# Kernel tuning notes

Measured on AMD Instinct MI355X. Metric: run time of the kernel, lower is better.

## Reference

```python
import jax, jax.numpy as jnp
import numpy as np
import math

B, S, D, H, FF, L = 8, 1024, 1024, 8, 4096, 2
DK = D // H
NEG = -1e32
EPS = 1e-5


def _cosine_pe(seq_len, d_model):
    pos = jnp.arange(seq_len, dtype=jnp.float32)[:, None]
    div = jnp.exp(jnp.arange(0, d_model, 2, dtype=jnp.float32) * (-(math.log(10000.0) / d_model)))
    pe = jnp.zeros((seq_len, d_model), dtype=jnp.float32)
    pe = pe.at[:, 0::2].set(jnp.sin(pos * div))
    pe = pe.at[:, 1::2].set(jnp.cos(pos * div))
    return pe


def setup_inputs() -> dict:
    key = jax.random.key(0)
    ks = jax.random.split(key, 12)
    sc = 0.02
    g = lambda k, shape: (jax.random.normal(k, shape, jnp.float32) * sc)
    return {
        "q_embed": jax.random.normal(ks[0], (B, S, D), jnp.float32),
        "qa_embed": jax.random.normal(ks[1], (B, S, D), jnp.float32),
        "pos_emb": _cosine_pe(S, D),
        "Wk": g(ks[2], (L, D, D)), "bk": jnp.zeros((L, D), jnp.float32),
        "Wv": g(ks[3], (L, D, D)), "bv": jnp.zeros((L, D), jnp.float32),
        "Wo": g(ks[4], (L, D, D)), "bo": jnp.zeros((L, D), jnp.float32),
        "ln1_g": jnp.ones((L, D), jnp.float32), "ln1_b": jnp.zeros((L, D), jnp.float32),
        "W1": g(ks[5], (L, FF, D)), "b1": jnp.zeros((L, FF), jnp.float32),
        "W2": g(ks[6], (L, D, FF)), "b2": jnp.zeros((L, D), jnp.float32),
        "ln2_g": jnp.ones((L, D), jnp.float32), "ln2_b": jnp.zeros((L, D), jnp.float32),
    }


def _layernorm(x, g, b):
    m = jnp.mean(x, axis=-1, keepdims=True)
    v = jnp.mean(jnp.square(x - m), axis=-1, keepdims=True)
    return (x - m) * jax.lax.rsqrt(v + EPS) * g + b


def _mha(x, y, Wk, bk, Wv, bv, Wo, bo, allow):
    # kq_same=1: q and k both come from k_linear applied to x (query==key input)
    k = (jnp.einsum('bsd,od->bso', x, Wk) + bk).reshape(B, S, H, DK).transpose(0, 2, 1, 3)
    q = k  # identical projection and identical input
    v = (jnp.einsum('bsd,od->bso', y, Wv) + bv).reshape(B, S, H, DK).transpose(0, 2, 1, 3)
    scores = jnp.einsum('bhqd,bhkd->bhqk', q, k) / math.sqrt(DK)
    scores = jnp.where(allow, scores, NEG)  # masked_fill(mask==0, -1e32)
    attn = jax.nn.softmax(scores, axis=-1)
    attn = attn.at[:, :, 0, :].set(0.0)  # zero_pad: first query row zeroed
    out = jnp.einsum('bhqk,bhkd->bhqd', attn, v)
    out = out.transpose(0, 2, 1, 3).reshape(B, S, D)
    return jnp.einsum('bsd,od->bso', out, Wo) + bo


def reference(q_embed, qa_embed, pos_emb, Wk, bk, Wv, bv, Wo, bo,
              ln1_g, ln1_b, W1, b1, W2, b2, ln2_g, ln2_b):
    x = q_embed + pos_emb[None]
    y = qa_embed + pos_emb[None]
    # strictly-lower-triangular allowed positions (triu(k=0)==0)
    allow = jnp.tril(jnp.ones((S, S), dtype=bool), -1)[None, None]
    for l in range(L):
        q2 = _mha(x, x, y, Wk[l], bk[l], Wv[l], bv[l], Wo[l], bo[l], allow) if False else _mha(x, y, Wk[l], bk[l], Wv[l], bv[l], Wo[l], bo[l], allow)
        x = _layernorm(x + q2, ln1_g[l], ln1_b[l])
        ff = jnp.einsum('bsf,df->bsd', jax.nn.relu(jnp.einsum('bsd,fd->bsf', x, W1[l]) + b1[l]), W2[l]) + b2[l]
        x = _layernorm(x + ff, ln2_g[l], ln2_b[l])
    return x
```

## Files before the change

### kernel.cpp

```cpp
#include <hip/hip_runtime.h>
#include <hip/hip_bf16.h>
#include <cstdint>
#include <cstddef>

#define B_  8
#define S_  1024
#define D_  1024
#define H_  8
#define FF_ 4096
#define L_  2
#define DK_ 128

typedef __bf16 bf16x8 __attribute__((ext_vector_type(8)));
typedef float  f32x4  __attribute__((ext_vector_type(4)));

__device__ __forceinline__ unsigned short f2bf(float f) {
    union { float f; uint32_t u; } v; v.f = f;
    uint32_t r = v.u + 0x7fffu + ((v.u >> 16) & 1u);
    return (unsigned short)(r >> 16);
}
__device__ __forceinline__ float bf2f(unsigned short u) {
    union { uint32_t u; float f; } v; v.u = ((uint32_t)u) << 16; return v.f;
}

__global__ __launch_bounds__(256) void init_xy(
    const float* __restrict__ qe, const float* __restrict__ qa,
    const float* __restrict__ pe,
    unsigned short* __restrict__ xb, unsigned short* __restrict__ yb)
{
    int i = (blockIdx.x * 256 + threadIdx.x) * 4;
    int pi = i & (S_ * D_ - 1);
    float4 q = *(const float4*)(qe + i);
    float4 a = *(const float4*)(qa + i);
    float4 p = *(const float4*)(pe + pi);
    ushort4 xo; xo.x = f2bf(q.x + p.x); xo.y = f2bf(q.y + p.y);
    xo.z = f2bf(q.z + p.z); xo.w = f2bf(q.w + p.w);
    ushort4 yo; yo.x = f2bf(a.x + p.x); yo.y = f2bf(a.y + p.y);
    yo.z = f2bf(a.z + p.z); yo.w = f2bf(a.w + p.w);
    *(ushort4*)(xb + i) = xo;
    *(ushort4*)(yb + i) = yo;
}

__global__ __launch_bounds__(256) void cvt_bf16(
    const float* __restrict__ in, unsigned short* __restrict__ out)
{
    int i = (blockIdx.x * 256 + threadIdx.x) * 4;
    float4 f = *(const float4*)(in + i);
    ushort4 o; o.x = f2bf(f.x); o.y = f2bf(f.y); o.z = f2bf(f.z); o.w = f2bf(f.w);
    *(ushort4*)(out + i) = o;
}

template<bool RELU, int OMODE>
__global__ __launch_bounds__(256) void gemm_bt(
    const unsigned short* __restrict__ A, const unsigned short* __restrict__ W,
    const float* __restrict__ bias, void* __restrict__ Cout,
    int M, int N, int K)
{
    __shared__ unsigned short sA[2][128][64];
    __shared__ unsigned short sW[2][128][64];

    const int tid  = threadIdx.x;
    const int lane = tid & 63;
    const int w    = tid >> 6;
    const int l16  = lane & 15;
    const int quad = lane >> 4;
    const int m0 = blockIdx.y * 128;
    const int n0 = blockIdx.x * 128;
    const int rw = (w >> 1) * 64;
    const int cw = (w & 1) * 64;

    const int srow   = lane >> 3;
    const int schunk = lane & 7;

    auto stage = [&](int k0, int buf) {
        #pragma unroll
        for (int i = 0; i < 4; ++i) {
            int r0  = w * 32 + i * 8;
            int row = r0 + srow;
            int gc  = schunk ^ (row & 7);
            const unsigned short* ga = A + (size_t)(m0 + row) * K + k0 + gc * 8;
            const unsigned short* gw = W + (size_t)(n0 + row) * K + k0 + gc * 8;
            __builtin_amdgcn_global_load_lds(
                (const __attribute__((address_space(1))) unsigned int*)ga,
                (__attribute__((address_space(3))) unsigned int*)&sA[buf][r0][0], 16, 0, 0);
            __builtin_amdgcn_global_load_lds(
                (const __attribute__((address_space(1))) unsigned int*)gw,
                (__attribute__((address_space(3))) unsigned int*)&sW[buf][r0][0], 16, 0, 0);
        }
    };

    f32x4 acc[4][4] = {};
    const int NK = K >> 6;
    int cur = 0;
    stage(0, 0);

    for (int kt = 0; kt < NK; ++kt) {
        __syncthreads();
        if (kt + 1 < NK) stage((kt + 1) << 6, cur ^ 1);

        #pragma unroll
        for (int ks = 0; ks < 2; ++ks) {
            bf16x8 af[4], wf[4];
            #pragma unroll
            for (int t = 0; t < 4; ++t) {
                int arow = rw + t * 16 + l16;
                int achk = (ks * 4 + quad) ^ (arow & 7);
                af[t] = *(const bf16x8*)&sA[cur][arow][achk * 8];
                int wrow = cw + t * 16 + l16;
                int wchk = (ks * 4 + quad) ^ (wrow & 7);
                wf[t] = *(const bf16x8*)&sW[cur][wrow][wchk * 8];
            }
            #pragma unroll
            for (int it = 0; it < 4; ++it)
                #pragma unroll
                for (int jt = 0; jt < 4; ++jt)
                    acc[it][jt] = __builtin_amdgcn_mfma_f32_16x16x32_bf16(
                        af[it], wf[jt], acc[it][jt], 0, 0, 0);
        }
        cur ^= 1;
    }

    #pragma unroll
    for (int it = 0; it < 4; ++it)
        #pragma unroll
        for (int jt = 0; jt < 4; ++jt) {
            int row = m0 + rw + it * 16 + quad * 4;
            int col = n0 + cw + jt * 16 + l16;
            float bcol = bias[col];
            float v[4];
            #pragma unroll
            for (int r = 0; r < 4; ++r) {
                v[r] = acc[it][jt][r] + bcol;
                if (RELU) v[r] = fmaxf(v[r], 0.0f);
            }
            if (OMODE == 1) {
                #pragma unroll
                for (int r = 0; r < 4; ++r)
                    ((unsigned short*)Cout)[(size_t)(row + r) * N + col] = f2bf(v[r]);
            } else {
                int key = row & (S_ - 1);
                int bb  = row >> 10;
                int hh  = col >> 7, dim = col & (DK_ - 1);
                unsigned short* dst = (unsigned short*)Cout
                    + ((size_t)(bb * H_ + hh) * DK_ + dim) * S_ + key;
                ushort4 o4; o4.x = f2bf(v[0]); o4.y = f2bf(v[1]);
                o4.z = f2bf(v[2]); o4.w = f2bf(v[3]);
                *(ushort4*)dst = o4;
            }
        }
}

template<bool RELU>
__global__ __launch_bounds__(512, 2) void gemm_bt8(
    const unsigned short* __restrict__ A, const unsigned short* __restrict__ W,
    const float* __restrict__ bias, unsigned short* __restrict__ Cout,
    int M, int N, int K)
{
    __shared__ unsigned short sA[2][256][64];
    __shared__ unsigned short sB[2][256][64];

    const int tid  = threadIdx.x;
    const int lane = tid & 63;
    const int w    = tid >> 6;
    const int l16  = lane & 15;
    const int quad = lane >> 4;
    const int wr   = w >> 2;
    const int wc   = w & 3;

    const int nwg = gridDim.x * gridDim.y;
    const int bid = blockIdx.y * gridDim.x + blockIdx.x;
    const int sb  = (bid & 7) * (nwg >> 3) + (bid >> 3);
    const int m0  = (sb / gridDim.x) * 256;
    const int n0  = (sb % gridDim.x) * 256;

    const int srow8 = lane >> 3;
    const int schk  = (lane & 7) ^ srow8;

    auto stA = [&](int i, int buf, int k0) {
        int r0 = i * 64 + w * 8;
        const unsigned short* g = A + (size_t)(m0 + r0 + srow8) * K + k0 + schk * 8;
        __builtin_amdgcn_global_load_lds(
            (const __attribute__((address_space(1))) unsigned int*)g,
            (__attribute__((address_space(3))) unsigned int*)&sA[buf][r0][0], 16, 0, 0);
    };
    auto stB = [&](int i, int buf, int k0) {
        int r0 = i * 64 + w * 8;
        const unsigned short* g = W + (size_t)(n0 + r0 + srow8) * K + k0 + schk * 8;
        __builtin_amdgcn_global_load_lds(
            (const __attribute__((address_space(1))) unsigned int*)g,
            (__attribute__((address_space(3))) unsigned int*)&sB[buf][r0][0], 16, 0, 0);
    };
    auto rdA = [&](int buf, int t, int ks) {
        int row = wr * 128 + t * 16 + l16;
        int chk = (ks * 4 + quad) ^ (row & 7);
        return *(const bf16x8*)&sA[buf][row][chk * 8];
    };
    auto rdB = [&](int buf, int j, int ks) {
        int row = wc * 64 + j * 16 + l16;
        int chk = (ks * 4 + quad) ^ (row & 7);
        return *(const bf16x8*)&sB[buf][row][chk * 8];
    };

    f32x4 acc[8][4] = {};
    const int NK = K >> 6;
    int cur = 0;

    stB(0, 0, 0); stB(1, 0, 0); stB(2, 0, 0); stB(3, 0, 0);
    stA(0, 0, 0); stA(2, 0, 0); stA(1, 0, 0); stA(3, 0, 0);
    asm volatile("s_waitcnt vmcnt(2)\n\ts_barrier" ::: "memory");

    for (int kt = 0; kt < NK; ++kt) {
        const bool pref = (kt + 1 < NK);
        const int  k1   = (kt + 1) << 6;
        const int  nb   = cur ^ 1;
        bf16x8 bfr[2][4];
        bf16x8 a0, a1, a2, a3;

        #pragma unroll
        for (int ks = 0; ks < 2; ++ks)
            #pragma unroll
            for (int j = 0; j < 4; ++j) bfr[ks][j] = rdB(cur, j, ks);
        a0 = rdA(cur, 0, 0); a1 = rdA(cur, 0, 1);
        a2 = rdA(cur, 1, 0); a3 = rdA(cur, 1, 1);
        if (pref) { stB(0, nb, k1); stB(1, nb, k1); }
        __builtin_amdgcn_s_setprio(1);
        #pragma unroll
        for (int j = 0; j < 4; ++j) {
            acc[0][j] = __builtin_amdgcn_mfma_f32_16x16x32_bf16(a0, bfr[0][j], acc[0][j], 0, 0, 0);
            acc[1][j] = __builtin_amdgcn_mfma_f32_16x16x32_bf16(a2, bfr[0][j], acc[1][j], 0, 0, 0);
        }
        #pragma unroll
        for (int j = 0; j < 4; ++j) {
            acc[0][j] = __builtin_amdgcn_mfma_f32_16x16x32_bf16(a1, bfr[1][j], acc[0][j], 0, 0, 0);
            acc[1][j] = __builtin_amdgcn_mfma_f32_16x16x32_bf16(a3, bfr[1][j], acc[1][j], 0, 0, 0);
        }
        __builtin_amdgcn_s_setprio(0);
        asm volatile("s_barrier" ::: "memory");

        a0 = rdA(cur, 2, 0); a1 = rdA(cur, 2, 1);
        a2 = rdA(cur, 3, 0); a3 = rdA(cur, 3, 1);
        if (pref) { stB(2, nb, k1); stB(3, nb, k1); }
        __builtin_amdgcn_s_setprio(1);
        #pragma unroll
        for (int j = 0; j < 4; ++j) {
            acc[2][j] = __builtin_amdgcn_mfma_f32_16x16x32_bf16(a0, bfr[0][j], acc[2][j], 0, 0, 0);
            acc[3][j] = __builtin_amdgcn_mfma_f32_16x16x32_bf16(a2, bfr[0][j], acc[3][j], 0, 0, 0);
        }
        #pragma unroll
        for (int j = 0; j < 4; ++j) {
            acc[2][j] = __builtin_amdgcn_mfma_f32_16x16x32_bf16(a1, bfr[1][j], acc[2][j], 0, 0, 0);
            acc[3][j] = __builtin_amdgcn_mfma_f32_16x16x32_bf16(a3, bfr[1][j], acc[3][j], 0, 0, 0);
        }
        __builtin_amdgcn_s_setprio(0);
        if (pref) asm volatile("s_waitcnt vmcnt(4)\n\ts_barrier" ::: "memory");
        else      asm volatile("s_waitcnt vmcnt(0)\n\ts_barrier" ::: "memory");

        a0 = rdA(cur, 4, 0); a1 = rdA(cur, 4, 1);
        a2 = rdA(cur, 5, 0); a3 = rdA(cur, 5, 1);
        if (pref) { stA(0, nb, k1); stA(2, nb, k1); }
        __builtin_amdgcn_s_setprio(1);
        #pragma unroll
        for (int j = 0; j < 4; ++j) {
            acc[4][j] = __builtin_amdgcn_mfma_f32_16x16x32_bf16(a0, bfr[0][j], acc[4][j], 0, 0, 0);
            acc[5][j] = __builtin_amdgcn_mfma_f32_16x16x32_bf16(a2, bfr[0][j], acc[5][j], 0, 0, 0);
        }
        #pragma unroll
        for (int j = 0; j < 4; ++j) {
            acc[4][j] = __builtin_amdgcn_mfma_f32_16x16x32_bf16(a1, bfr[1][j], acc[4][j], 0, 0, 0);
            acc[5][j] = __builtin_amdgcn_mfma_f32_16x16x32_bf16(a3, bfr[1][j], acc[5][j], 0, 0, 0);
        }
        __builtin_amdgcn_s_setprio(0);
        asm volatile("s_barrier" ::: "memory");

        a0 = rdA(cur, 6, 0); a1 = rdA(cur, 6, 1);
        a2 = rdA(cur, 7, 0); a3 = rdA(cur, 7, 1);
        if (pref) { stA(1, nb, k1); stA(3, nb, k1); }
        __builtin_amdgcn_s_setprio(1);
        #pragma unroll
        for (int j = 0; j < 4; ++j) {
            acc[6][j] = __builtin_amdgcn_mfma_f32_16x16x32_bf16(a0, bfr[0][j], acc[6][j], 0, 0, 0);
            acc[7][j] = __builtin_amdgcn_mfma_f32_16x16x32_bf16(a2, bfr[0][j], acc[7][j], 0, 0, 0);
        }
        #pragma unroll
        for (int j = 0; j < 4; ++j) {
            acc[6][j] = __builtin_amdgcn_mfma_f32_16x16x32_bf16(a1, bfr[1][j], acc[6][j], 0, 0, 0);
            acc[7][j] = __builtin_amdgcn_mfma_f32_16x16x32_bf16(a3, bfr[1][j], acc[7][j], 0, 0, 0);
        }
        __builtin_amdgcn_s_setprio(0);
        asm volatile("s_waitcnt vmcnt(2)\n\ts_barrier" ::: "memory");
        cur = nb;
    }

    #pragma unroll
    for (int t = 0; t < 8; ++t)
        #pragma unroll
        for (int j = 0; j < 4; ++j) {
            int row = m0 + wr * 128 + t * 16 + quad * 4;
            int col = n0 + wc * 64 + j * 16 + l16;
            float bcol = bias[col];
            #pragma unroll
            for (int r = 0; r < 4; ++r) {
                float v = acc[t][j][r] + bcol;
                if (RELU) v = fmaxf(v, 0.0f);
                Cout[(size_t)(row + r) * N + col] = f2bf(v);
            }
        }
}

__global__ __launch_bounds__(256) void attn_mfma(
    const unsigned short* __restrict__ Kbuf, const unsigned short* __restrict__ Vtbuf,
    unsigned short* __restrict__ Obuf)
{
    __shared__ unsigned short sK[2][64][128];
    __shared__ unsigned short sVt[2][128][64];
    __shared__ unsigned short sP[4][16][72];

    const int tid  = threadIdx.x;
    const int lane = tid & 63;
    const int w    = tid >> 6;
    const int l16  = lane & 15;
    const int quad = lane >> 4;
    const int pa   = blockIdx.x;
    const int bh   = blockIdx.y;
    const int b    = bh >> 3, h = bh & 7;
    const unsigned short* KB  = Kbuf  + ((size_t)b * S_) * D_ + h * DK_;
    const unsigned short* VTB = Vtbuf + (size_t)bh * DK_ * S_;

    const float scale = 0.08838834764831845f;

    auto stage = [&](int kt, int buf) {
        #pragma unroll
        for (int i = 0; i < 4; ++i) {
            int r0  = w * 16 + i * 4;
            int row = r0 + (lane >> 4);
            int c   = (lane & 15) ^ (row & 15);
            const unsigned short* g = KB + (size_t)(kt * 64 + row) * D_ + c * 8;
            __builtin_amdgcn_global_load_lds(
                (const __attribute__((address_space(1))) unsigned int*)g,
                (__attribute__((address_space(3))) unsigned int*)&sK[buf][r0][0], 16, 0, 0);
        }
        #pragma unroll
        for (int i = 0; i < 4; ++i) {
            int r0  = w * 32 + i * 8;
            int row = r0 + (lane >> 3);
            int c   = (lane & 7) ^ (row & 7);
            const unsigned short* g = VTB + (size_t)row * S_ + kt * 64 + c * 8;
            __builtin_amdgcn_global_load_lds(
                (const __attribute__((address_space(1))) unsigned int*)g,
                (__attribute__((address_space(3))) unsigned int*)&sVt[buf][r0][0], 16, 0, 0);
        }
    };

    #pragma unroll
    for (int half = 0; half < 2; ++half) {
        const int qt = half == 0 ? (15 - pa) : pa;
        const int q0 = qt * 64;

        bf16x8 qf[4];
        {
            const unsigned short* qrow = KB + (size_t)(q0 + w * 16 + l16) * D_ + quad * 8;
            #pragma unroll
            for (int ks = 0; ks < 4; ++ks)
                qf[ks] = *(const bf16x8*)(qrow + ks * 32);
        }

        f32x4 Oacc[8] = {};
        float m_run[4] = {-1e30f, -1e30f, -1e30f, -1e30f};
        float l_run[4] = {};

        int cur = 0;
        stage(0, cur);

        for (int kt = 0; kt <= qt; ++kt) {
            __syncthreads();
            if (kt < qt) stage(kt + 1, cur ^ 1);

            f32x4 sacc[4];
            #pragma unroll
            for (int nt = 0; nt < 4; ++nt) {
                f32x4 a = {};
                #pragma unroll
                for (int ks = 0; ks < 4; ++ks) {
                    int kr = nt * 16 + l16;
                    int p  = (ks * 4 + quad) ^ (kr & 15);
                    bf16x8 kf = *(const bf16x8*)&sK[cur][kr][p * 8];
                    a = __builtin_amdgcn_mfma_f32_16x16x32_bf16(qf[ks], kf, a, 0, 0, 0);
                }
                sacc[nt] = a;
            }

            const bool diag = (kt == qt);
            #pragma unroll
            for (int nt = 0; nt < 4; ++nt)
                #pragma unroll
                for (int r = 0; r < 4; ++r) {
                    float v = sacc[nt][r] * scale;
                    if (diag) {
                        int nidx = nt * 16 + l16;
                        int midx = w * 16 + quad * 4 + r;
                        if (nidx >= midx) v = -1e30f;
                    }
                    sacc[nt][r] = v;
                }

            float alpha[4];
            #pragma unroll
            for (int r = 0; r < 4; ++r) {
                float mx = fmaxf(fmaxf(sacc[0][r], sacc[1][r]), fmaxf(sacc[2][r], sacc[3][r]));
                mx = fmaxf(mx, __shfl_xor(mx, 1));
                mx = fmaxf(mx, __shfl_xor(mx, 2));
                mx = fmaxf(mx, __shfl_xor(mx, 4));
                mx = fmaxf(mx, __shfl_xor(mx, 8));
                float mn = fmaxf(m_run[r], mx);
                alpha[r] = __expf(m_run[r] - mn);
                m_run[r] = mn;
            }
            #pragma unroll
            for (int r = 0; r < 4; ++r) {
                float rs = 0.0f;
                #pragma unroll
                for (int nt = 0; nt < 4; ++nt) {
                    float e = __expf(sacc[nt][r] - m_run[r]);
                    sacc[nt][r] = e;
                    rs += e;
                }
                rs += __shfl_xor(rs, 1);
                rs += __shfl_xor(rs, 2);
                rs += __shfl_xor(rs, 4);
                rs += __shfl_xor(rs, 8);
                l_run[r] = l_run[r] * alpha[r] + rs;
            }
            #pragma unroll
            for (int o = 0; o < 8; ++o)
                #pragma unroll
                for (int r = 0; r < 4; ++r)
                    Oacc[o][r] *= alpha[r];

            #pragma unroll
            for (int nt = 0; nt < 4; ++nt)
                #pragma unroll
                for (int r = 0; r < 4; ++r)
                    sP[w][quad * 4 + r][nt * 16 + l16] = f2bf(sacc[nt][r]);

            bf16x8 pf[2];
            #pragma unroll
            for (int ks = 0; ks < 2; ++ks)
                pf[ks] = *(const bf16x8*)&sP[w][l16][ks * 32 + quad * 8];
            #pragma unroll
            for (int nt = 0; nt < 8; ++nt) {
                #pragma unroll
                for (int ks = 0; ks < 2; ++ks) {
                    int vr = nt * 16 + l16;
                    int p  = (ks * 4 + quad) ^ (vr & 7);
                    bf16x8 vf = *(const bf16x8*)&sVt[cur][vr][p * 8];
                    Oacc[nt] = __builtin_amdgcn_mfma_f32_16x16x32_bf16(pf[ks], vf, Oacc[nt], 0, 0, 0);
                }
            }
            cur ^= 1;
        }

        float inv[4];
        #pragma unroll
        for (int r = 0; r < 4; ++r) {
            int m = q0 + w * 16 + quad * 4 + r;
            inv[r] = (l_run[r] > 0.0f && m != 0) ? 1.0f / l_run[r] : 0.0f;
        }
        #pragma unroll
        for (int nt = 0; nt < 8; ++nt)
            #pragma unroll
            for (int r = 0; r < 4; ++r) {
                int m = q0 + w * 16 + quad * 4 + r;
                Obuf[((size_t)b * S_ + m) * D_ + h * DK_ + nt * 16 + l16] =
                    f2bf(Oacc[nt][r] * inv[r]);
            }
    }
}

template<bool FINAL>
__global__ __launch_bounds__(256) void ln_res(
    const unsigned short* __restrict__ xin, const unsigned short* __restrict__ delta,
    const float* __restrict__ g, const float* __restrict__ bta,
    unsigned short* __restrict__ xbout, float* __restrict__ fout)
{
    __shared__ float red1[4], red2[4];
    const int row = blockIdx.x;
    const int tid = threadIdx.x;
    const int c = tid * 4;
    ushort4 xu = *(const ushort4*)(xin + (size_t)row * D_ + c);
    ushort4 du = *(const ushort4*)(delta + (size_t)row * D_ + c);
    float t0 = bf2f(xu.x) + bf2f(du.x), t1 = bf2f(xu.y) + bf2f(du.y);
    float t2 = bf2f(xu.z) + bf2f(du.z), t3 = bf2f(xu.w) + bf2f(du.w);

    float s = t0 + t1 + t2 + t3;
    #pragma unroll
    for (int off = 32; off > 0; off >>= 1) s += __shfl_down(s, off);
    if ((tid & 63) == 0) red1[tid >> 6] = s;
    __syncthreads();
    float mean = (red1[0] + red1[1] + red1[2] + red1[3]) * (1.0f / 1024.0f);

    float e0 = t0 - mean, e1 = t1 - mean, e2 = t2 - mean, e3 = t3 - mean;
    float ss = e0 * e0 + e1 * e1 + e2 * e2 + e3 * e3;
    #pragma unroll
    for (int off = 32; off > 0; off >>= 1) ss += __shfl_down(ss, off);
    if ((tid & 63) == 0) red2[tid >> 6] = ss;
    __syncthreads();
    float var = (red2[0] + red2[1] + red2[2] + red2[3]) * (1.0f / 1024.0f);
    float rstd = rsqrtf(var + 1e-5f);

    float4 gv = *(const float4*)(g + c);
    float4 bv = *(const float4*)(bta + c);
    float o0 = e0 * rstd * gv.x + bv.x;
    float o1 = e1 * rstd * gv.y + bv.y;
    float o2 = e2 * rstd * gv.z + bv.z;
    float o3 = e3 * rstd * gv.w + bv.w;
    if (FINAL) {
        *(float4*)(fout + (size_t)row * D_ + c) = make_float4(o0, o1, o2, o3);
    } else {
        ushort4 ob; ob.x = f2bf(o0); ob.y = f2bf(o1); ob.z = f2bf(o2); ob.w = f2bf(o3);
        *(ushort4*)(xbout + (size_t)row * D_ + c) = ob;
    }
}

extern "C" void kernel_launch(void* const* d_in, const int* in_sizes, int n_in,
                              void* d_out, int out_size, void* d_ws, size_t ws_size,
                              hipStream_t stream)
{
    const float* qe   = (const float*)d_in[0];
    const float* qa   = (const float*)d_in[1];
    const float* pe   = (const float*)d_in[2];
    const float* Wk   = (const float*)d_in[3];
    const float* bk   = (const float*)d_in[4];
    const float* Wv   = (const float*)d_in[5];
    const float* bv   = (const float*)d_in[6];
    const float* Wo   = (const float*)d_in[7];
    const float* bo   = (const float*)d_in[8];
    const float* ln1g = (const float*)d_in[9];
    const float* ln1b = (const float*)d_in[10];
    const float* W1   = (const float*)d_in[11];
    const float* b1   = (const float*)d_in[12];
    const float* W2   = (const float*)d_in[13];
    const float* b2   = (const float*)d_in[14];
    const float* ln2g = (const float*)d_in[15];
    const float* ln2b = (const float*)d_in[16];

    const size_t BSD = (size_t)B_ * S_ * D_;
    const size_t BSF = (size_t)B_ * S_ * FF_;
    const size_t WDD = (size_t)D_ * D_;
    const size_t WFD = (size_t)FF_ * D_;

    char* p = (char*)d_ws;
    auto take = [&](size_t bytes) { char* r = p; p += (bytes + 255) & ~255ULL; return r; };
    unsigned short* xb    = (unsigned short*)take(BSD * 2);
    unsigned short* yb    = (unsigned short*)take(BSD * 2);
    unsigned short* delta = (unsigned short*)take(BSD * 2);
    char*           uni   = take(BSF * 2);
    unsigned short* Kb    = (unsigned short*)uni;
    unsigned short* Vt    = Kb + BSD;
    unsigned short* attnb = Vt + BSD;
    unsigned short* hb    = (unsigned short*)uni;
    unsigned short* wslot = (unsigned short*)take(WFD * 2);

    init_xy<<<(int)(BSD / 4 / 256), 256, 0, stream>>>(qe, qa, pe, xb, yb);

    const int M = B_ * S_;
    for (int l = 0; l < L_; ++l) {
        cvt_bf16<<<(int)(WDD / 1024), 256, 0, stream>>>(Wk + l * WDD, wslot);
        gemm_bt<false, 1><<<dim3(D_ / 128, M / 128), 256, 0, stream>>>(
            xb, wslot, bk + l * D_, Kb, M, D_, D_);
        cvt_bf16<<<(int)(WDD / 1024), 256, 0, stream>>>(Wv + l * WDD, wslot);
        gemm_bt<false, 2><<<dim3(D_ / 128, M / 128), 256, 0, stream>>>(
            yb, wslot, bv + l * D_, Vt, M, D_, D_);
        attn_mfma<<<dim3(8, B_ * H_), 256, 0, stream>>>(Kb, Vt, attnb);
        cvt_bf16<<<(int)(WDD / 1024), 256, 0, stream>>>(Wo + l * WDD, wslot);
        gemm_bt<false, 1><<<dim3(D_ / 128, M / 128), 256, 0, stream>>>(
            attnb, wslot, bo + l * D_, delta, M, D_, D_);
        ln_res<false><<<M, 256, 0, stream>>>(xb, delta, ln1g + l * D_, ln1b + l * D_, xb, nullptr);
        cvt_bf16<<<(int)(WFD / 1024), 256, 0, stream>>>(W1 + l * WFD, wslot);
        gemm_bt8<true><<<dim3(FF_ / 256, M / 256), 512, 0, stream>>>(
            xb, wslot, b1 + l * FF_, hb, M, FF_, D_);
        cvt_bf16<<<(int)(WFD / 1024), 256, 0, stream>>>(W2 + l * WFD, wslot);
        gemm_bt<false, 1><<<dim3(D_ / 128, M / 128), 256, 0, stream>>>(
            hb, wslot, b2 + l * D_, delta, M, D_, FF_);
        if (l == L_ - 1)
            ln_res<true><<<M, 256, 0, stream>>>(xb, delta, ln2g + l * D_, ln2b + l * D_,
                                               nullptr, (float*)d_out);
        else
            ln_res<false><<<M, 256, 0, stream>>>(xb, delta, ln2g + l * D_, ln2b + l * D_,
                                                xb, nullptr);
    }
}
```

Measured before the change: 830.1 us.

## Replace 128x128 GEMM with 256x128 pipelined 8-wave kernel for N=1024 projections

Adds a gemm_btn kernel that uses a 256x128 tile with 8 waves, split-phase prefetch via global_load_lds, s_setprio around the MFMA bursts, and XCD-aware block swizzling. It replaces the older 128x128 4-wave gemm_bt for the K, V, O and W2 projections, keeping the transposed V output mode. The aim is more reuse per LDS load and better overlap of loads with MFMA on the N=1024 GEMMs. The cost is that the grid shrinks to 256 blocks, which may underfill the CUs.

Result: slower. 872.5 us (+5.1%).

```diff
diff --git a/kernel.cpp b/kernel.cpp
--- a/kernel.cpp
+++ b/kernel.cpp
@@ -50,89 +50,314 @@
     *(ushort4*)(out + i) = o;
 }
 
-template<bool RELU, int OMODE>
-__global__ __launch_bounds__(256) void gemm_bt(
+template<bool RELU>
+__global__ __launch_bounds__(512, 2) void gemm_bt8(
     const unsigned short* __restrict__ A, const unsigned short* __restrict__ W,
-    const float* __restrict__ bias, void* __restrict__ Cout,
+    const float* __restrict__ bias, unsigned short* __restrict__ Cout,
     int M, int N, int K)
 {
-    __shared__ unsigned short sA[2][128][64];
-    __shared__ unsigned short sW[2][128][64];
+    __shared__ unsigned short sA[2][256][64];
+    __shared__ unsigned short sB[2][256][64];
 
     const int tid  = threadIdx.x;
     const int lane = tid & 63;
     const int w    = tid >> 6;
     const int l16  = lane & 15;
     const int quad = lane >> 4;
-    const int m0 = blockIdx.y * 128;
-    const int n0 = blockIdx.x * 128;
-    const int rw = (w >> 1) * 64;
-    const int cw = (w & 1) * 64;
-
-    const int srow   = lane >> 3;
-    const int schunk = lane & 7;
-
-    auto stage = [&](int k0, int buf) {
-        #pragma unroll
-        for (int i = 0; i < 4; ++i) {
-            int r0  = w * 32 + i * 8;
-            int row = r0 + srow;
-            int gc  = schunk ^ (row & 7);
-            const unsigned short* ga = A + (size_t)(m0 + row) * K + k0 + gc * 8;
-            const unsigned short* gw = W + (size_t)(n0 + row) * K + k0 + gc * 8;
-            __builtin_amdgcn_global_load_lds(
-                (const __attribute__((address_space(1))) unsigned int*)ga,
-                (__attribute__((address_space(3))) unsigned int*)&sA[buf][r0][0], 16, 0, 0);
-            __builtin_amdgcn_global_load_lds(
-                (const __attribute__((address_space(1))) unsigned int*)gw,
-                (__attribute__((address_space(3))) unsigned int*)&sW[buf][r0][0], 16, 0, 0);
-        }
-    };
-
-    f32x4 acc[4][4] = {};
+    const int wr   = w >> 2;
+    const int wc   = w & 3;
+
+    const int nwg = gridDim.x * gridDim.y;
+    const int bid = blockIdx.y * gridDim.x + blockIdx.x;
+    const int sb  = (bid & 7) * (nwg >> 3) + (bid >> 3);
+    const int m0  = (sb / gridDim.x) * 256;
+    const int n0  = (sb % gridDim.x) * 256;
+
+    const int srow8 = lane >> 3;
+    const int schk  = (lane & 7) ^ srow8;
+
+    auto stA = [&](int i, int buf, int k0) {
+        int r0 = i * 64 + w * 8;
+        const unsigned short* g = A + (size_t)(m0 + r0 + srow8) * K + k0 + schk * 8;
+        __builtin_amdgcn_global_load_lds(
+            (const __attribute__((address_space(1))) unsigned int*)g,
+            (__attribute__((address_space(3))) unsigned int*)&sA[buf][r0][0], 16, 0, 0);
+    };
+    auto stB = [&](int i, int buf, int k0) {
+        int r0 = i * 64 + w * 8;
+        const unsigned short* g = W + (size_t)(n0 + r0 + srow8) * K + k0 + schk * 8;
+        __builtin_amdgcn_global_load_lds(
+            (const __attribute__((address_space(1))) unsigned int*)g,
+            (__attribute__((address_space(3))) unsigned int*)&sB[buf][r0][0], 16, 0, 0);
+    };
+    auto rdA = [&](int buf, int t, int ks) {
+        int row = wr * 128 + t * 16 + l16;
+        int chk = (ks * 4 + quad) ^ (row & 7);
+        return *(const bf16x8*)&sA[buf][row][chk * 8];
+    };
+    auto rdB = [&](int buf, int j, int ks) {
+        int row = wc * 64 + j * 16 + l16;
+        int chk = (ks * 4 + quad) ^ (row & 7);
+        return *(const bf16x8*)&sB[buf][row][chk * 8];
+    };
+
+    f32x4 acc[8][4] = {};
     const int NK = K >> 6;
     int cur = 0;
-    stage(0, 0);
+
+    stB(0, 0, 0); stB(1, 0, 0); stB(2, 0, 0); stB(3, 0, 0);
+    stA(0, 0, 0); stA(2, 0, 0); stA(1, 0, 0); stA(3, 0, 0);
+    asm volatile("s_waitcnt vmcnt(2)\n\ts_barrier" ::: "memory");
 
     for (int kt = 0; kt < NK; ++kt) {
-        __syncthreads();
-        if (kt + 1 < NK) stage((kt + 1) << 6, cur ^ 1);
-
-        #pragma unroll
-        for (int ks = 0; ks < 2; ++ks) {
-            bf16x8 af[4], wf[4];
-            #pragma unroll
-            for (int t = 0; t < 4; ++t) {
-                int arow = rw + t * 16 + l16;
-                int achk = (ks * 4 + quad) ^ (arow & 7);
-                af[t] = *(const bf16x8*)&sA[cur][arow][achk * 8];
-                int wrow = cw + t * 16 + l16;
-                int wchk = (ks * 4 + quad) ^ (wrow & 7);
-                wf[t] = *(const bf16x8*)&sW[cur][wrow][wchk * 8];
+        const bool pref = (kt + 1 < NK);
+        const int  k1   = (kt + 1) << 6;
+        const int  nb   = cur ^ 1;
+        bf16x8 bfr[2][4];
+        bf16x8 a0, a1, a2, a3;
+
+        #pragma unroll
+        for (int ks = 0; ks < 2; ++ks)
+            #pragma unroll
+            for (int j = 0; j < 4; ++j) bfr[ks][j] = rdB(cur, j, ks);
+        a0 = rdA(cur, 0, 0); a1 = rdA(cur, 0, 1);
+        a2 = rdA(cur, 1, 0); a3 = rdA(cur, 1, 1);
+        if (pref) { stB(0, nb, k1); stB(1, nb, k1); }
+        __builtin_amdgcn_s_setprio(1);
+        #pragma unroll
+        for (int j = 0; j < 4; ++j) {
+            acc[0][j] = __builtin_amdgcn_mfma_f32_16x16x32_bf16(a0, bfr[0][j], acc[0][j], 0, 0, 0);
+            acc[1][j] = __builtin_amdgcn_mfma_f32_16x16x32_bf16(a2, bfr[0][j], acc[1][j], 0, 0, 0);
+        }
+        #pragma unroll
+        for (int j = 0; j < 4; ++j) {
+            acc[0][j] = __builtin_amdgcn_mfma_f32_16x16x32_bf16(a1, bfr[1][j], acc[0][j], 0, 0, 0);
+            acc[1][j] = __builtin_amdgcn_mfma_f32_16x16x32_bf16(a3, bfr[1][j], acc[1][j], 0, 0, 0);
+        }
+        __builtin_amdgcn_s_setprio(0);
+        asm volatile("s_barrier" ::: "memory");
+
+        a0 = rdA(cur, 2, 0); a1 = rdA(cur, 2, 1);
+        a2 = rdA(cur, 3, 0); a3 = rdA(cur, 3, 1);
+        if (pref) { stB(2, nb, k1); stB(3, nb, k1); }
+        __builtin_amdgcn_s_setprio(1);
+        #pragma unroll
+        for (int j = 0; j < 4; ++j) {
+            acc[2][j] = __builtin_amdgcn_mfma_f32_16x16x32_bf16(a0, bfr[0][j], acc[2][j], 0, 0, 0);
+            acc[3][j] = __builtin_amdgcn_mfma_f32_16x16x32_bf16(a2, bfr[0][j], acc[3][j], 0, 0, 0);
+        }
+        #pragma unroll
+        for (int j = 0; j < 4; ++j) {
+            acc[2][j] = __builtin_amdgcn_mfma_f32_16x16x32_bf16(a1, bfr[1][j], acc[2][j], 0, 0, 0);
+            acc[3][j] = __builtin_amdgcn_mfma_f32_16x16x32_bf16(a3, bfr[1][j], acc[3][j], 0, 0, 0);
+        }
+        __builtin_amdgcn_s_setprio(0);
+        if (pref) asm volatile("s_waitcnt vmcnt(4)\n\ts_barrier" ::: "memory");
+        else      asm volatile("s_waitcnt vmcnt(0)\n\ts_barrier" ::: "memory");
+
+        a0 = rdA(cur, 4, 0); a1 = rdA(cur, 4, 1);
+        a2 = rdA(cur, 5, 0); a3 = rdA(cur, 5, 1);
+        if (pref) { stA(0, nb, k1); stA(2, nb, k1); }
+        __builtin_amdgcn_s_setprio(1);
+        #pragma unroll
+        for (int j = 0; j < 4; ++j) {
+            acc[4][j] = __builtin_amdgcn_mfma_f32_16x16x32_bf16(a0, bfr[0][j], acc[4][j], 0, 0, 0);
+            acc[5][j] = __builtin_amdgcn_mfma_f32_16x16x32_bf16(a2, bfr[0][j], acc[5][j], 0, 0, 0);
+        }
+        #pragma unroll
+        for (int j = 0; j < 4; ++j) {
+            acc[4][j] = __builtin_amdgcn_mfma_f32_16x16x32_bf16(a1, bfr[1][j], acc[4][j], 0, 0, 0);
+            acc[5][j] = __builtin_amdgcn_mfma_f32_16x16x32_bf16(a3, bfr[1][j], acc[5][j], 0, 0, 0);
+        }
+        __builtin_amdgcn_s_setprio(0);
+        asm volatile("s_barrier" ::: "memory");
+
+        a0 = rdA(cur, 6, 0); a1 = rdA(cur, 6, 1);
+        a2 = rdA(cur, 7, 0); a3 = rdA(cur, 7, 1);
+        if (pref) { stA(1, nb, k1); stA(3, nb, k1); }
+        __builtin_amdgcn_s_setprio(1);
+        #pragma unroll
+        for (int j = 0; j < 4; ++j) {
+            acc[6][j] = __builtin_amdgcn_mfma_f32_16x16x32_bf16(a0, bfr[0][j], acc[6][j], 0, 0, 0);
+            acc[7][j] = __builtin_amdgcn_mfma_f32_16x16x32_bf16(a2, bfr[0][j], acc[7][j], 0, 0, 0);
+        }
+        #pragma unroll
+        for (int j = 0; j < 4; ++j) {
+            acc[6][j] = __builtin_amdgcn_mfma_f32_16x16x32_bf16(a1, bfr[1][j], acc[6][j], 0, 0, 0);
+            acc[7][j] = __builtin_amdgcn_mfma_f32_16x16x32_bf16(a3, bfr[1][j], acc[7][j], 0, 0, 0);
+        }
+        __builtin_amdgcn_s_setprio(0);
+        asm volatile("s_waitcnt vmcnt(2)\n\ts_barrier" ::: "memory");
+        cur = nb;
+    }
+
+    #pragma unroll
+    for (int t = 0; t < 8; ++t)
+        #pragma unroll
+        for (int j = 0; j < 4; ++j) {
+            int row = m0 + wr * 128 + t * 16 + quad * 4;
+            int col = n0 + wc * 64 + j * 16 + l16;
+            float bcol = bias[col];
+            #pragma unroll
+            for (int r = 0; r < 4; ++r) {
+                float v = acc[t][j][r] + bcol;
+                if (RELU) v = fmaxf(v, 0.0f);
+                Cout[(size_t)(row + r) * N + col] = f2bf(v);
             }
-            #pragma unroll
-            for (int it = 0; it < 4; ++it)
-                #pragma unroll
-                for (int jt = 0; jt < 4; ++jt)
-                    acc[it][jt] = __builtin_amdgcn_mfma_f32_16x16x32_bf16(
-                        af[it], wf[jt], acc[it][jt], 0, 0, 0);
-        }
-        cur ^= 1;
+        }
+}
+
+template<int OMODE>
+__global__ __launch_bounds__(512, 2) void gemm_btn(
+    const unsigned short* __restrict__ A, const unsigned short* __restrict__ W,
+    const float* __restrict__ bias, void* __restrict__ Cout,
+    int M, int N, int K)
+{
+    __shared__ unsigned short sA[2][256][64];
+    __shared__ unsigned short sB[2][128][64];
+
+    const int tid  = threadIdx.x;
+    const int lane = tid & 63;
+    const int w    = tid >> 6;
+    const int l16  = lane & 15;
+    const int quad = lane >> 4;
+    const int wr   = w >> 2;
+    const int wc   = w & 3;
+
+    const int nwg = gridDim.x * gridDim.y;
+    const int bid = blockIdx.y * gridDim.x + blockIdx.x;
+    const int sb  = (bid & 7) * (nwg >> 3) + (bid >> 3);
+    const int m0  = (sb / gridDim.x) * 256;
+    const int n0  = (sb % gridDim.x) * 128;
+
+    const int srow8 = lane >> 3;
+    const int schk  = (lane & 7) ^ srow8;
+
+    auto stA = [&](int i, int buf, int k0) {
+        int r0 = i * 64 + w * 8;
+        const unsigned short* g = A + (size_t)(m0 + r0 + srow8) * K + k0 + schk * 8;
+        __builtin_amdgcn_global_load_lds(
+            (const __attribute__((address_space(1))) unsigned int*)g,
+            (__attribute__((address_space(3))) unsigned int*)&sA[buf][r0][0], 16, 0, 0);
+    };
+    auto stB = [&](int i, int buf, int k0) {
+        int r0 = i * 64 + w * 8;
+        const unsigned short* g = W + (size_t)(n0 + r0 + srow8) * K + k0 + schk * 8;
+        __builtin_amdgcn_global_load_lds(
+            (const __attribute__((address_space(1))) unsigned int*)g,
+            (__attribute__((address_space(3))) unsigned int*)&sB[buf][r0][0], 16, 0, 0);
+    };
+    auto rdA = [&](int buf, int t, int ks) {
+        int row = wr * 128 + t * 16 + l16;
+        int chk = (ks * 4 + quad) ^ (row & 7);
+        return *(const bf16x8*)&sA[buf][row][chk * 8];
+    };
+    auto rdB = [&](int buf, int j, int ks) {
+        int row = wc * 32 + j * 16 + l16;
+        int chk = (ks * 4 + quad) ^ (row & 7);
+        return *(const bf16x8*)&sB[buf][row][chk * 8];
+    };
+
+    f32x4 acc[8][2] = {};
+    const int NK = K >> 6;
+    int cur = 0;
+
+    stB(0, 0, 0); stB(1, 0, 0);
+    stA(0, 0, 0); stA(2, 0, 0);
+    stA(1, 0, 0); stA(3, 0, 0);
+    asm volatile("s_waitcnt vmcnt(2)\n\ts_barrier" ::: "memory");
+
+    for (int kt = 0; kt < NK; ++kt) {
+        const bool pref = (kt + 1 < NK);
+        const int  k1   = (kt + 1) << 6;
+        const int  nb   = cur ^ 1;
+        bf16x8 bfr[2][2];
+        bf16x8 a0, a1, a2, a3;
+
+        #pragma unroll
+        for (int ks = 0; ks < 2; ++ks)
+            #pragma unroll
+            for (int j = 0; j < 2; ++j) bfr[ks][j] = rdB(cur, j, ks);
+        a0 = rdA(cur, 0, 0); a1 = rdA(cur, 0, 1);
+        a2 = rdA(cur, 1, 0); a3 = rdA(cur, 1, 1);
+        if (pref) { stB(0, nb, k1); stB(1, nb, k1); }
+        __builtin_amdgcn_s_setprio(1);
+        #pragma unroll
+        for (int j = 0; j < 2; ++j) {
+            acc[0][j] = __builtin_amdgcn_mfma_f32_16x16x32_bf16(a0, bfr[0][j], acc[0][j], 0, 0, 0);
+            acc[1][j] = __builtin_amdgcn_mfma_f32_16x16x32_bf16(a2, bfr[0][j], acc[1][j], 0, 0, 0);
+        }
+        #pragma unroll
+        for (int j = 0; j < 2; ++j) {
+            acc[0][j] = __builtin_amdgcn_mfma_f32_16x16x32_bf16(a1, bfr[1][j], acc[0][j], 0, 0, 0);
+            acc[1][j] = __builtin_amdgcn_mfma_f32_16x16x32_bf16(a3, bfr[1][j], acc[1][j], 0, 0, 0);
+        }
+        __builtin_amdgcn_s_setprio(0);
+        asm volatile("s_barrier" ::: "memory");
+
+        a0 = rdA(cur, 2, 0); a1 = rdA(cur, 2, 1);
+        a2 = rdA(cur, 3, 0); a3 = rdA(cur, 3, 1);
+        if (pref) { stA(0, nb, k1); stA(2, nb, k1); }
+        __builtin_amdgcn_s_setprio(1);
+        #pragma unroll
+        for (int j = 0; j < 2; ++j) {
+            acc[2][j] = __builtin_amdgcn_mfma_f32_16x16x32_bf16(a0, bfr[0][j], acc[2][j], 0, 0, 0);
+            acc[3][j] = __builtin_amdgcn_mfma_f32_16x16x32_bf16(a2, bfr[0][j], acc[3][j], 0, 0, 0);
+        }
+        #pragma unroll
+        for (int j = 0; j < 2; ++j) {
+            acc[2][j] = __builtin_amdgcn_mfma_f32_16x16x32_bf16(a1, bfr[1][j], acc[2][j], 0, 0, 0);
+            acc[3][j] = __builtin_amdgcn_mfma_f32_16x16x32_bf16(a3, bfr[1][j], acc[3][j], 0, 0, 0);
+        }
+        __builtin_amdgcn_s_setprio(0);
+        if (pref) asm volatile("s_waitcnt vmcnt(4)\n\ts_barrier" ::: "memory");
+        else      asm volatile("s_waitcnt vmcnt(0)\n\ts_barrier" ::: "memory");
+
+        a0 = rdA(cur, 4, 0); a1 = rdA(cur, 4, 1);
+        a2 = rdA(cur, 5, 0); a3 = rdA(cur, 5, 1);
+        if (pref) { stA(1, nb, k1); stA(3, nb, k1); }
+        __builtin_amdgcn_s_setprio(1);
+        #pragma unroll
+        for (int j = 0; j < 2; ++j) {
+            acc[4][j] = __builtin_amdgcn_mfma_f32_16x16x32_bf16(a0, bfr[0][j], acc[4][j], 0, 0, 0);
+            acc[5][j] = __builtin_amdgcn_mfma_f32_16x16x32_bf16(a2, bfr[0][j], acc[5][j], 0, 0, 0);
+        }
+        #pragma unroll
+        for (int j = 0; j < 2; ++j) {
+            acc[4][j] = __builtin_amdgcn_mfma_f32_16x16x32_bf16(a1, bfr[1][j], acc[4][j], 0, 0, 0);
+            acc[5][j] = __builtin_amdgcn_mfma_f32_16x16x32_bf16(a3, bfr[1][j], acc[5][j], 0, 0, 0);
+        }
+        __builtin_amdgcn_s_setprio(0);
+        asm volatile("s_barrier" ::: "memory");
+
+        a0 = rdA(cur, 6, 0); a1 = rdA(cur, 6, 1);
+        a2 = rdA(cur, 7, 0); a3 = rdA(cur, 7, 1);
+        __builtin_amdgcn_s_setprio(1);
+        #pragma unroll
+        for (int j = 0; j < 2; ++j) {
+            acc[6][j] = __builtin_amdgcn_mfma_f32_16x16x32_bf16(a0, bfr[0][j], acc[6][j], 0, 0, 0);
+            acc[7][j] = __builtin_amdgcn_mfma_f32_16x16x32_bf16(a2, bfr[0][j], acc[7][j], 0, 0, 0);
+        }
+        #pragma unroll
+        for (int j = 0; j < 2; ++j) {
+            acc[6][j] = __builtin_amdgcn_mfma_f32_16x16x32_bf16(a1, bfr[1][j], acc[6][j], 0, 0, 0);
+            acc[7][j] = __builtin_amdgcn_mfma_f32_16x16x32_bf16(a3, bfr[1][j], acc[7][j], 0, 0, 0);
+        }
+        __builtin_amdgcn_s_setprio(0);
+        asm volatile("s_waitcnt vmcnt(2)\n\ts_barrier" ::: "memory");
+        cur = nb;
     }
 
     #pragma unroll
-    for (int it = 0; it < 4; ++it)
-        #pragma unroll
-        for (int jt = 0; jt < 4; ++jt) {
-            int row = m0 + rw + it * 16 + quad * 4;
-            int col = n0 + cw + jt * 16 + l16;
+    for (int t = 0; t < 8; ++t)
+        #pragma unroll
+        for (int j = 0; j < 2; ++j) {
+            int row = m0 + wr * 128 + t * 16 + quad * 4;
+            int col = n0 + wc * 32 + j * 16 + l16;
             float bcol = bias[col];
             float v[4];
             #pragma unroll
-            for (int r = 0; r < 4; ++r) {
-                v[r] = acc[it][jt][r] + bcol;
-                if (RELU) v[r] = fmaxf(v[r], 0.0f);
-            }
+            for (int r = 0; r < 4; ++r) v[r] = acc[t][j][r] + bcol;
             if (OMODE == 1) {
                 #pragma unroll
                 for (int r = 0; r < 4; ++r)
@@ -146,163 +371,6 @@
                 ushort4 o4; o4.x = f2bf(v[0]); o4.y = f2bf(v[1]);
                 o4.z = f2bf(v[2]); o4.w = f2bf(v[3]);
                 *(ushort4*)dst = o4;
-            }
-        }
-}
-
-template<bool RELU>
-__global__ __launch_bounds__(512, 2) void gemm_bt8(
-    const unsigned short* __restrict__ A, const unsigned short* __restrict__ W,
-    const float* __restrict__ bias, unsigned short* __restrict__ Cout,
-    int M, int N, int K)
-{
-    __shared__ unsigned short sA[2][256][64];
-    __shared__ unsigned short sB[2][256][64];
-
-    const int tid  = threadIdx.x;
-    const int lane = tid & 63;
-    const int w    = tid >> 6;
-    const int l16  = lane & 15;
-    const int quad = lane >> 4;
-    const int wr   = w >> 2;
-    const int wc   = w & 3;
-
-    const int nwg = gridDim.x * gridDim.y;
-    const int bid = blockIdx.y * gridDim.x + blockIdx.x;
-    const int sb  = (bid & 7) * (nwg >> 3) + (bid >> 3);
-    const int m0  = (sb / gridDim.x) * 256;
-    const int n0  = (sb % gridDim.x) * 256;
-
-    const int srow8 = lane >> 3;
-    const int schk  = (lane & 7) ^ srow8;
-
-    auto stA = [&](int i, int buf, int k0) {
-        int r0 = i * 64 + w * 8;
-        const unsigned short* g = A + (size_t)(m0 + r0 + srow8) * K + k0 + schk * 8;
-        __builtin_amdgcn_global_load_lds(
-            (const __attribute__((address_space(1))) unsigned int*)g,
-            (__attribute__((address_space(3))) unsigned int*)&sA[buf][r0][0], 16, 0, 0);
-    };
-    auto stB = [&](int i, int buf, int k0) {
-        int r0 = i * 64 + w * 8;
-        const unsigned short* g = W + (size_t)(n0 + r0 + srow8) * K + k0 + schk * 8;
-        __builtin_amdgcn_global_load_lds(
-            (const __attribute__((address_space(1))) unsigned int*)g,
-            (__attribute__((address_space(3))) unsigned int*)&sB[buf][r0][0], 16, 0, 0);
-    };
-    auto rdA = [&](int buf, int t, int ks) {
-        int row = wr * 128 + t * 16 + l16;
-        int chk = (ks * 4 + quad) ^ (row & 7);
-        return *(const bf16x8*)&sA[buf][row][chk * 8];
-    };
-    auto rdB = [&](int buf, int j, int ks) {
-        int row = wc * 64 + j * 16 + l16;
-        int chk = (ks * 4 + quad) ^ (row & 7);
-        return *(const bf16x8*)&sB[buf][row][chk * 8];
-    };
-
-    f32x4 acc[8][4] = {};
-    const int NK = K >> 6;
-    int cur = 0;
-
-    stB(0, 0, 0); stB(1, 0, 0); stB(2, 0, 0); stB(3, 0, 0);
-    stA(0, 0, 0); stA(2, 0, 0); stA(1, 0, 0); stA(3, 0, 0);
-    asm volatile("s_waitcnt vmcnt(2)\n\ts_barrier" ::: "memory");
-
-    for (int kt = 0; kt < NK; ++kt) {
-        const bool pref = (kt + 1 < NK);
-        const int  k1   = (kt + 1) << 6;
-        const int  nb   = cur ^ 1;
-        bf16x8 bfr[2][4];
-        bf16x8 a0, a1, a2, a3;
-
-        #pragma unroll
-        for (int ks = 0; ks < 2; ++ks)
-            #pragma unroll
-            for (int j = 0; j < 4; ++j) bfr[ks][j] = rdB(cur, j, ks);
-        a0 = rdA(cur, 0, 0); a1 = rdA(cur, 0, 1);
-        a2 = rdA(cur, 1, 0); a3 = rdA(cur, 1, 1);
-        if (pref) { stB(0, nb, k1); stB(1, nb, k1); }
-        __builtin_amdgcn_s_setprio(1);
-        #pragma unroll
-        for (int j = 0; j < 4; ++j) {
-            acc[0][j] = __builtin_amdgcn_mfma_f32_16x16x32_bf16(a0, bfr[0][j], acc[0][j], 0, 0, 0);
-            acc[1][j] = __builtin_amdgcn_mfma_f32_16x16x32_bf16(a2, bfr[0][j], acc[1][j], 0, 0, 0);
-        }
-        #pragma unroll
-        for (int j = 0; j < 4; ++j) {
-            acc[0][j] = __builtin_amdgcn_mfma_f32_16x16x32_bf16(a1, bfr[1][j], acc[0][j], 0, 0, 0);
-            acc[1][j] = __builtin_amdgcn_mfma_f32_16x16x32_bf16(a3, bfr[1][j], acc[1][j], 0, 0, 0);
-        }
-        __builtin_amdgcn_s_setprio(0);
-        asm volatile("s_barrier" ::: "memory");
-
-        a0 = rdA(cur, 2, 0); a1 = rdA(cur, 2, 1);
-        a2 = rdA(cur, 3, 0); a3 = rdA(cur, 3, 1);
-        if (pref) { stB(2, nb, k1); stB(3, nb, k1); }
-        __builtin_amdgcn_s_setprio(1);
-        #pragma unroll
-        for (int j = 0; j < 4; ++j) {
-            acc[2][j] = __builtin_amdgcn_mfma_f32_16x16x32_bf16(a0, bfr[0][j], acc[2][j], 0, 0, 0);
-            acc[3][j] = __builtin_amdgcn_mfma_f32_16x16x32_bf16(a2, bfr[0][j], acc[3][j], 0, 0, 0);
-        }
-        #pragma unroll
-        for (int j = 0; j < 4; ++j) {
-            acc[2][j] = __builtin_amdgcn_mfma_f32_16x16x32_bf16(a1, bfr[1][j], acc[2][j], 0, 0, 0);
-            acc[3][j] = __builtin_amdgcn_mfma_f32_16x16x32_bf16(a3, bfr[1][j], acc[3][j], 0, 0, 0);
-        }
-        __builtin_amdgcn_s_setprio(0);
-        if (pref) asm volatile("s_waitcnt vmcnt(4)\n\ts_barrier" ::: "memory");
-        else      asm volatile("s_waitcnt vmcnt(0)\n\ts_barrier" ::: "memory");
-
-        a0 = rdA(cur, 4, 0); a1 = rdA(cur, 4, 1);
-        a2 = rdA(cur, 5, 0); a3 = rdA(cur, 5, 1);
-        if (pref) { stA(0, nb, k1); stA(2, nb, k1); }
-        __builtin_amdgcn_s_setprio(1);
-        #pragma unroll
-        for (int j = 0; j < 4; ++j) {
-            acc[4][j] = __builtin_amdgcn_mfma_f32_16x16x32_bf16(a0, bfr[0][j], acc[4][j], 0, 0, 0);
-            acc[5][j] = __builtin_amdgcn_mfma_f32_16x16x32_bf16(a2, bfr[0][j], acc[5][j], 0, 0, 0);
-        }
-        #pragma unroll
-        for (int j = 0; j < 4; ++j) {
-            acc[4][j] = __builtin_amdgcn_mfma_f32_16x16x32_bf16(a1, bfr[1][j], acc[4][j], 0, 0, 0);
-            acc[5][j] = __builtin_amdgcn_mfma_f32_16x16x32_bf16(a3, bfr[1][j], acc[5][j], 0, 0, 0);
-        }
-        __builtin_amdgcn_s_setprio(0);
-        asm volatile("s_barrier" ::: "memory");
-
-        a0 = rdA(cur, 6, 0); a1 = rdA(cur, 6, 1);
-        a2 = rdA(cur, 7, 0); a3 = rdA(cur, 7, 1);
-        if (pref) { stA(1, nb, k1); stA(3, nb, k1); }
-        __builtin_amdgcn_s_setprio(1);
-        #pragma unroll
-        for (int j = 0; j < 4; ++j) {
-            acc[6][j] = __builtin_amdgcn_mfma_f32_16x16x32_bf16(a0, bfr[0][j], acc[6][j], 0, 0, 0);
-            acc[7][j] = __builtin_amdgcn_mfma_f32_16x16x32_bf16(a2, bfr[0][j], acc[7][j], 0, 0, 0);
-        }
-        #pragma unroll
-        for (int j = 0; j < 4; ++j) {
-            acc[6][j] = __builtin_amdgcn_mfma_f32_16x16x32_bf16(a1, bfr[1][j], acc[6][j], 0, 0, 0);
-            acc[7][j] = __builtin_amdgcn_mfma_f32_16x16x32_bf16(a3, bfr[1][j], acc[7][j], 0, 0, 0);
-        }
-        __builtin_amdgcn_s_setprio(0);
-        asm volatile("s_waitcnt vmcnt(2)\n\ts_barrier" ::: "memory");
-        cur = nb;
-    }
-
-    #pragma unroll
-    for (int t = 0; t < 8; ++t)
-        #pragma unroll
-        for (int j = 0; j < 4; ++j) {
-            int row = m0 + wr * 128 + t * 16 + quad * 4;
-            int col = n0 + wc * 64 + j * 16 + l16;
-            float bcol = bias[col];
-            #pragma unroll
-            for (int r = 0; r < 4; ++r) {
-                float v = acc[t][j][r] + bcol;
-                if (RELU) v = fmaxf(v, 0.0f);
-                Cout[(size_t)(row + r) * N + col] = f2bf(v);
             }
         }
 }
@@ -565,21 +633,21 @@
     const int M = B_ * S_;
     for (int l = 0; l < L_; ++l) {
         cvt_bf16<<<(int)(WDD / 1024), 256, 0, stream>>>(Wk + l * WDD, wslot);
-        gemm_bt<false, 1><<<dim3(D_ / 128, M / 128), 256, 0, stream>>>(
+        gemm_btn<1><<<dim3(D_ / 128, M / 256), 512, 0, stream>>>(
             xb, wslot, bk + l * D_, Kb, M, D_, D_);
         cvt_bf16<<<(int)(WDD / 1024), 256, 0, stream>>>(Wv + l * WDD, wslot);
-        gemm_bt<false, 2><<<dim3(D_ / 128, M / 128), 256, 0, stream>>>(
+        gemm_btn<2><<<dim3(D_ / 128, M / 256), 512, 0, stream>>>(
             yb, wslot, bv + l * D_, Vt, M, D_, D_);
         attn_mfma<<<dim3(8, B_ * H_), 256, 0, stream>>>(Kb, Vt, attnb);
         cvt_bf16<<<(int)(WDD / 1024), 256, 0, stream>>>(Wo + l * WDD, wslot);
-        gemm_bt<false, 1><<<dim3(D_ / 128, M / 128), 256, 0, stream>>>(
+        gemm_btn<1><<<dim3(D_ / 128, M / 256), 512, 0, stream>>>(
             attnb, wslot, bo + l * D_, delta, M, D_, D_);
         ln_res<false><<<M, 256, 0, stream>>>(xb, delta, ln1g + l * D_, ln1b + l * D_, xb, nullptr);
         cvt_bf16<<<(int)(WFD / 1024), 256, 0, stream>>>(W1 + l * WFD, wslot);
         gemm_bt8<true><<<dim3(FF_ / 256, M / 256), 512, 0, stream>>>(
             xb, wslot, b1 + l * FF_, hb, M, FF_, D_);
         cvt_bf16<<<(int)(WFD / 1024), 256, 0, stream>>>(W2 + l * WFD, wslot);
-        gemm_bt<false, 1><<<dim3(D_ / 128, M / 128), 256, 0, stream>>>(
+        gemm_btn<1><<<dim3(D_ / 128, M / 256), 512, 0, stream>>>(
             hb, wslot, b2 + l * D_, delta, M, D_, FF_);
         if (l == L_ - 1)
             ln_res<true><<<M, 256, 0, stream>>>(xb, delta, ln2g + l * D_, ln2b + l * D_,
```
